# Optimization experiments

Hardware: AMD Instinct MI355X
Metric: run time of the kernel (lower is better)

## Reference

```python
import jax, jax.numpy as jnp
import numpy as np

N = 50000   # num_nodes
T = 24      # window_size
H = 64      # hidden_dim
HOR = 12    # horizon
E = 1600000 # num edges


def setup_inputs() -> dict:
    key = jax.random.key(0)
    ks = jax.random.split(key, 12)
    s = 1.0 / np.sqrt(H)
    u = lambda k, shape: jax.random.uniform(k, shape, jnp.float32, -s, s)
    return {
        "x": jax.random.normal(ks[0], (N, T), jnp.float32),
        "edge_index": jax.random.randint(ks[1], (2, E), 0, N, dtype=jnp.int32),
        "w_ih": u(ks[2], (3 * H, 1)),
        "w_hh": u(ks[3], (3 * H, H)),
        "b_ih": u(ks[4], (3 * H,)),
        "b_hh": u(ks[5], (3 * H,)),
        "gc1_w": u(ks[6], (H, H)),
        "gc1_b": u(ks[7], (H,)),
        "gc2_w": u(ks[8], (H, H)),
        "gc2_b": u(ks[9], (H,)),
        "fc_w": u(ks[10], (HOR, H)),
        "fc_b": u(ks[11], (HOR,)),
    }


def _gru_last(x, w_ih, w_hh, b_ih, b_hh):
    # x: [N, T] scalar-per-step input (input_size=1). Returns final hidden [N, H].
    h0 = jnp.zeros((x.shape[0], H), x.dtype)

    def step(h, xt):  # xt: [N]
        gi = xt[:, None] * w_ih[:, 0][None, :] + b_ih   # [N, 3H]
        gh = h @ w_hh.T + b_hh                          # [N, 3H]
        i_r, i_z, i_n = jnp.split(gi, 3, axis=-1)
        h_r, h_z, h_n = jnp.split(gh, 3, axis=-1)
        r = jax.nn.sigmoid(i_r + h_r)
        z = jax.nn.sigmoid(i_z + h_z)
        n = jnp.tanh(i_n + r * h_n)
        h = (1.0 - z) * n + z * h
        return h, None

    hT, _ = jax.lax.scan(step, h0, x.T)  # scan over time axis
    return hT


def _gcn_norm(edge_index, n):
    # PyG GCNConv: add self loops, symmetric D^-1/2 (A+I) D^-1/2 normalization.
    loops = jnp.arange(n, dtype=edge_index.dtype)
    src = jnp.concatenate([edge_index[0], loops])
    dst = jnp.concatenate([edge_index[1], loops])
    deg = jax.ops.segment_sum(jnp.ones(src.shape, jnp.float32), dst, num_segments=n)
    dinv = jnp.where(deg > 0, jax.lax.rsqrt(jnp.maximum(deg, 1e-12)), 0.0)
    return src, dst, dinv[src] * dinv[dst]


def _gcn(h, src, dst, norm, W, b, n):
    hw = h @ W.T                      # [N, H] linear transform first
    msg = hw[src] * norm[:, None]     # gather + edge weighting
    return jax.ops.segment_sum(msg, dst, num_segments=n) + b


def reference(x, edge_index, w_ih, w_hh, b_ih, b_hh, gc1_w, gc1_b, gc2_w, gc2_b, fc_w, fc_b):
    n = x.shape[0]
    h = _gru_last(x, w_ih, w_hh, b_ih, b_hh)            # [N, H] last GRU output
    src, dst, norm = _gcn_norm(edge_index, n)
    h = jax.nn.relu(_gcn(h, src, dst, norm, gc1_w, gc1_b, n))
    h = jax.nn.relu(_gcn(h, src, dst, norm, gc2_w, gc2_b, n))
    return h @ fc_w.T + fc_b                            # [N, HOR]
```

## Files before the change

### kernel.cpp

```cpp
#include <hip/hip_runtime.h>

#define NN 50000
#define TT 24
#define HH 64
#define HORZ 12
#define EE 1600000

#define GP 256
#define EP (EE / GP)
#define BK 784
#define NBG (BK * GP)
#define SCB (NBG / 512)
#define BKA ((NN + 63) / 64)

typedef __attribute__((ext_vector_type(8))) _Float16 f16x8;
typedef __attribute__((ext_vector_type(4))) float f32x4;

__device__ __forceinline__ float sigm(float x) {
  return __builtin_amdgcn_rcpf(1.f + __expf(-x));
}
__device__ __forceinline__ float tanh_f(float x) {
  return 1.f - 2.f * __builtin_amdgcn_rcpf(1.f + __expf(2.f * x));
}

__global__ void build_frags_kernel(const float* __restrict__ whh, const float* __restrict__ g1,
                                   const float* __restrict__ g2, const float* __restrict__ fcw,
                                   _Float16* __restrict__ frag) {
  int idx = blockIdx.x * 256 + threadIdx.x;
  if (idx >= 21504) return;
  const float* W;
  int rows, li;
  if (idx < 12288) { W = whh; rows = 192; li = idx; }
  else if (idx < 16384) { W = g1; rows = 64; li = idx - 12288; }
  else if (idx < 20480) { W = g2; rows = 64; li = idx - 16384; }
  else { W = fcw; rows = HORZ; li = idx - 20480; }
  int j = li & 7;
  int l = (li >> 3) & 63;
  int kf = (li >> 9) & 1;
  int nf = li >> 10;
  int col = 16 * nf + (l & 15);
  int k = 32 * kf + 8 * (l >> 4) + j;
  frag[idx] = (col < rows) ? (_Float16)W[col * 64 + k] : (_Float16)0.f;
}

__global__ __launch_bounds__(256) void p1_hist_kernel(const int* __restrict__ dst,
                                                      int* __restrict__ hist) {
  __shared__ int h[BK];
  int tid = threadIdx.x, g = blockIdx.x;
  for (int b = tid; b < BK; b += 256) h[b] = 0;
  __syncthreads();
  int e0 = g * EP;
  for (int i = tid; i < EP; i += 256) atomicAdd(&h[dst[e0 + i] >> 6], 1);
  __syncthreads();
  for (int b = tid; b < BK; b += 256) hist[b * GP + g] = h[b];
}

__global__ void scanA_kernel(const int* __restrict__ v, int* __restrict__ part) {
  __shared__ int s[512];
  int i = blockIdx.x * 512 + threadIdx.x;
  s[threadIdx.x] = v[i];
  __syncthreads();
  for (int off = 256; off > 0; off >>= 1) {
    if (threadIdx.x < off) s[threadIdx.x] += s[threadIdx.x + off];
    __syncthreads();
  }
  if (threadIdx.x == 0) part[blockIdx.x] = s[0];
}

__global__ void scanB_kernel(int* __restrict__ part) {
  __shared__ int s[512];
  int t = threadIdx.x;
  int v = (t < SCB) ? part[t] : 0;
  s[t] = v;
  __syncthreads();
  for (int off = 1; off < 512; off <<= 1) {
    int a = s[t];
    int b = (t >= off) ? s[t - off] : 0;
    __syncthreads();
    s[t] = a + b;
    __syncthreads();
  }
  if (t < SCB) part[t] = s[t] - v;
}

__global__ void scanC_kernel(int* __restrict__ cellbase, const int* __restrict__ part) {
  __shared__ int s[2][512];
  int tid = threadIdx.x;
  int i = blockIdx.x * 512 + tid;
  int x = cellbase[i];
  s[0][tid] = x;
  __syncthreads();
  int cur = 0;
  for (int off = 1; off < 512; off <<= 1) {
    int nxt = cur ^ 1;
    int val = s[cur][tid] + ((tid >= off) ? s[cur][tid - off] : 0);
    s[nxt][tid] = val;
    __syncthreads();
    cur = nxt;
  }
  cellbase[i] = part[blockIdx.x] + s[cur][tid] - x;
  if (i == 0) cellbase[NBG] = EE;
}

__global__ __launch_bounds__(256) void p2_scatter_kernel(
    const int* __restrict__ src, const int* __restrict__ dst,
    const int* __restrict__ cellbase, unsigned int* __restrict__ rec) {
  __shared__ int cur[BK];
  int tid = threadIdx.x, g = blockIdx.x;
  for (int b = tid; b < BK; b += 256) cur[b] = cellbase[b * GP + g];
  __syncthreads();
  int e0 = g * EP;
  for (int i = tid; i < EP; i += 256) {
    int e = e0 + i;
    int d = dst[e];
    int s = src[e];
    int p = atomicAdd(&cur[d >> 6], 1);
    rec[p] = ((unsigned)(d & 63) << 16) | (unsigned)s;
  }
}

__global__ __launch_bounds__(256) void sort2_kernel(
    const unsigned int* __restrict__ rec, const int* __restrict__ cellbase,
    unsigned short* __restrict__ csr, int* __restrict__ row_start,
    float* __restrict__ dinv) {
  __shared__ int cnt[64];
  __shared__ int cur[64];
  int b = blockIdx.x, tid = threadIdx.x;
  if (tid < 64) cnt[tid] = 0;
  __syncthreads();
  int e0 = cellbase[b * GP], e1 = cellbase[(b + 1) * GP];
  for (int e = e0 + tid; e < e1; e += 256) atomicAdd(&cnt[rec[e] >> 16], 1);
  __syncthreads();
  if (tid == 0) {
    int a = e0;
#pragma unroll
    for (int l = 0; l < 64; ++l) { int c = cnt[l]; cur[l] = a; a += c; }
  }
  __syncthreads();
  if (tid < 64) {
    int n = b * 64 + tid;
    if (n <= NN) row_start[n] = cur[tid];
    if (n < NN) dinv[n] = rsqrtf((float)(cnt[tid] + 1));
  }
  __syncthreads();
  for (int e = e0 + tid; e < e1; e += 256) {
    unsigned int r = rec[e];
    int p = atomicAdd(&cur[r >> 16], 1);
    csr[p] = (unsigned short)(r & 0xFFFFu);
  }
}

__global__ __launch_bounds__(256, 8) void gru_kernel(
    const float* __restrict__ x, const float* __restrict__ w_ih,
    const float* __restrict__ b_ih, const float* __restrict__ b_hh,
    const _Float16* __restrict__ wfrag, const _Float16* __restrict__ l1f,
    const float* __restrict__ dinv, _Float16* __restrict__ hw) {
  __shared__ __align__(16) _Float16 sh[2][16][72];
  __shared__ __align__(16) float xs[TT][16];

  const int tid = threadIdx.x;
  const int lane = tid & 63;
  const int w = tid >> 6;
  const int c = lane & 15;
  const int q = lane >> 4;
  const int d = 16 * w + c;

  f16x8 Br0 = *(const f16x8*)&wfrag[(((w)*2 + 0) * 64 + lane) * 8];
  f16x8 Br1 = *(const f16x8*)&wfrag[(((w)*2 + 1) * 64 + lane) * 8];
  f16x8 Bz0 = *(const f16x8*)&wfrag[(((4 + w) * 2 + 0) * 64 + lane) * 8];
  f16x8 Bz1 = *(const f16x8*)&wfrag[(((4 + w) * 2 + 1) * 64 + lane) * 8];
  f16x8 Bn0 = *(const f16x8*)&wfrag[(((8 + w) * 2 + 0) * 64 + lane) * 8];
  f16x8 Bn1 = *(const f16x8*)&wfrag[(((8 + w) * 2 + 1) * 64 + lane) * 8];

  const float wir = w_ih[d], wiz = w_ih[64 + d], win = w_ih[128 + d];
  const float arb = b_ih[d] + b_hh[d];
  const float azb = b_ih[64 + d] + b_hh[64 + d];
  const float bin = b_ih[128 + d];
  const float bhn = b_hh[128 + d];

  const int base = blockIdx.x * 16;

  for (int i = tid; i < 16 * TT; i += 256) {
    int nl = i / TT;
    int t = i - nl * TT;
    xs[t][nl] = x[(base + nl) * TT + t];
  }
  __syncthreads();

  float hreg[4] = {0.f, 0.f, 0.f, 0.f};

#pragma unroll 1
  for (int tp = 0; tp < TT / 2; ++tp) {
#pragma unroll
    for (int half = 0; half < 2; ++half) {
      const int t = 2 * tp + half;
      f32x4 ar = (f32x4){arb, arb, arb, arb};
      f32x4 az = (f32x4){azb, azb, azb, azb};
      f32x4 an = (f32x4){bhn, bhn, bhn, bhn};
      if (t > 0) {
        const _Float16* S = &sh[half ^ 1][0][0];
        f16x8 a0 = *(const f16x8*)&S[c * 72 + 8 * q];
        f16x8 a1 = *(const f16x8*)&S[c * 72 + 32 + 8 * q];
        ar = __builtin_amdgcn_mfma_f32_16x16x32_f16(a0, Br0, ar, 0, 0, 0);
        az = __builtin_amdgcn_mfma_f32_16x16x32_f16(a0, Bz0, az, 0, 0, 0);
        an = __builtin_amdgcn_mfma_f32_16x16x32_f16(a0, Bn0, an, 0, 0, 0);
        ar = __builtin_amdgcn_mfma_f32_16x16x32_f16(a1, Br1, ar, 0, 0, 0);
        az = __builtin_amdgcn_mfma_f32_16x16x32_f16(a1, Bz1, az, 0, 0, 0);
        an = __builtin_amdgcn_mfma_f32_16x16x32_f16(a1, Bn1, an, 0, 0, 0);
      }
      float4 xt = *(const float4*)&xs[t][4 * q];
      float xv[4] = {xt.x, xt.y, xt.z, xt.w};
#pragma unroll
      for (int r = 0; r < 4; ++r) {
        float rg = sigm(xv[r] * wir + ar[r]);
        float zg = sigm(xv[r] * wiz + az[r]);
        float nn = tanh_f(rg * an[r] + (xv[r] * win + bin));
        float hn = nn + zg * (hreg[r] - nn);
        hreg[r] = hn;
        sh[half][4 * q + r][d] = (_Float16)hn;
      }
      __syncthreads();
    }
  }

  f16x8 L0 = *(const f16x8*)&l1f[((w * 2 + 0) * 64 + lane) * 8];
  f16x8 L1 = *(const f16x8*)&l1f[((w * 2 + 1) * 64 + lane) * 8];
  {
    const _Float16* S = &sh[1][0][0];
    f16x8 a0 = *(const f16x8*)&S[c * 72 + 8 * q];
    f16x8 a1 = *(const f16x8*)&S[c * 72 + 32 + 8 * q];
    f32x4 acc = (f32x4){0.f, 0.f, 0.f, 0.f};
    acc = __builtin_amdgcn_mfma_f32_16x16x32_f16(a0, L0, acc, 0, 0, 0);
    acc = __builtin_amdgcn_mfma_f32_16x16x32_f16(a1, L1, acc, 0, 0, 0);
#pragma unroll
    for (int r = 0; r < 4; ++r) {
      int n = base + 4 * q + r;
      hw[n * 64 + d] = (_Float16)(acc[r] * dinv[n]);
    }
  }
}

__global__ __launch_bounds__(1024, 4) void agg_lin_kernel(
    const _Float16* __restrict__ hwp, const float* __restrict__ dinv,
    const int* __restrict__ row_start, const unsigned short* __restrict__ csr,
    const float* __restrict__ bias, const _Float16* __restrict__ l2f,
    _Float16* __restrict__ out) {
  __shared__ __align__(16) _Float16 h1[64][72];
  int tid = threadIdx.x, b = blockIdx.x;
  int wv = tid >> 6, lane = tid & 63;
  float bl = bias[lane];
#pragma unroll 1
  for (int k = 0; k < 4; ++k) {
    int row = wv * 4 + k;
    int n = b * 64 + row;
    float v = 0.f;
    if (n < NN) {
      int e0 = row_start[n], e1 = row_start[n + 1];
      float a0 = (float)hwp[n * 64 + lane];
      float a1 = 0.f, a2 = 0.f, a3 = 0.f;
      int e = e0;
      for (; e < e1 && (e & 7); ++e) a0 += (float)hwp[(int)csr[e] * 64 + lane];
      for (; e + 8 <= e1; e += 8) {
        uint4 pk = *(const uint4*)&csr[e];
        a0 += (float)hwp[(pk.x & 0xFFFF) * 64 + lane];
        a1 += (float)hwp[(pk.x >> 16) * 64 + lane];
        a2 += (float)hwp[(pk.y & 0xFFFF) * 64 + lane];
        a3 += (float)hwp[(pk.y >> 16) * 64 + lane];
        a0 += (float)hwp[(pk.z & 0xFFFF) * 64 + lane];
        a1 += (float)hwp[(pk.z >> 16) * 64 + lane];
        a2 += (float)hwp[(pk.w & 0xFFFF) * 64 + lane];
        a3 += (float)hwp[(pk.w >> 16) * 64 + lane];
      }
      for (; e < e1; ++e) a0 += (float)hwp[(int)csr[e] * 64 + lane];
      v = (a0 + a1 + a2 + a3) * dinv[n] + bl;
      v = v > 0.f ? v : 0.f;
    }
    h1[row][lane] = (_Float16)v;
  }
  __syncthreads();
  int g = wv >> 2, wq = wv & 3;
  int c = lane & 15, q = lane >> 4;
  f16x8 B0 = *(const f16x8*)&l2f[((wq * 2 + 0) * 64 + lane) * 8];
  f16x8 B1 = *(const f16x8*)&l2f[((wq * 2 + 1) * 64 + lane) * 8];
  f16x8 a0 = *(const f16x8*)&h1[16 * g + c][8 * q];
  f16x8 a1 = *(const f16x8*)&h1[16 * g + c][32 + 8 * q];
  f32x4 acc = (f32x4){0.f, 0.f, 0.f, 0.f};
  acc = __builtin_amdgcn_mfma_f32_16x16x32_f16(a0, B0, acc, 0, 0, 0);
  acc = __builtin_amdgcn_mfma_f32_16x16x32_f16(a1, B1, acc, 0, 0, 0);
#pragma unroll
  for (int r = 0; r < 4; ++r) {
    int n = b * 64 + 16 * g + 4 * q + r;
    if (n < NN) out[n * 64 + 16 * wq + c] = (_Float16)(acc[r] * dinv[n]);
  }
}

__global__ __launch_bounds__(1024, 4) void agg_fc_kernel(
    const _Float16* __restrict__ hwp, const float* __restrict__ dinv,
    const int* __restrict__ row_start, const unsigned short* __restrict__ csr,
    const float* __restrict__ bias, const _Float16* __restrict__ fcf,
    const float* __restrict__ fcb, float* __restrict__ out) {
  __shared__ __align__(16) _Float16 h1[64][72];
  int tid = threadIdx.x, b = blockIdx.x;
  int wv = tid >> 6, lane = tid & 63;
  float bl = bias[lane];
#pragma unroll 1
  for (int k = 0; k < 4; ++k) {
    int row = wv * 4 + k;
    int n = b * 64 + row;
    float v = 0.f;
    if (n < NN) {
      int e0 = row_start[n], e1 = row_start[n + 1];
      float a0 = (float)hwp[n * 64 + lane];
      float a1 = 0.f, a2 = 0.f, a3 = 0.f;
      int e = e0;
      for (; e < e1 && (e & 7); ++e) a0 += (float)hwp[(int)csr[e] * 64 + lane];
      for (; e + 8 <= e1; e += 8) {
        uint4 pk = *(const uint4*)&csr[e];
        a0 += (float)hwp[(pk.x & 0xFFFF) * 64 + lane];
        a1 += (float)hwp[(pk.x >> 16) * 64 + lane];
        a2 += (float)hwp[(pk.y & 0xFFFF) * 64 + lane];
        a3 += (float)hwp[(pk.y >> 16) * 64 + lane];
        a0 += (float)hwp[(pk.z & 0xFFFF) * 64 + lane];
        a1 += (float)hwp[(pk.z >> 16) * 64 + lane];
        a2 += (float)hwp[(pk.w & 0xFFFF) * 64 + lane];
        a3 += (float)hwp[(pk.w >> 16) * 64 + lane];
      }
      for (; e < e1; ++e) a0 += (float)hwp[(int)csr[e] * 64 + lane];
      v = (a0 + a1 + a2 + a3) * dinv[n] + bl;
      v = v > 0.f ? v : 0.f;
    }
    h1[row][lane] = (_Float16)v;
  }
  __syncthreads();
  if (wv < 4) {
    int g = wv;
    int c = lane & 15, q = lane >> 4;
    f16x8 B0 = *(const f16x8*)&fcf[(0 * 64 + lane) * 8];
    f16x8 B1 = *(const f16x8*)&fcf[(1 * 64 + lane) * 8];
    f16x8 a0 = *(const f16x8*)&h1[16 * g + c][8 * q];
    f16x8 a1 = *(const f16x8*)&h1[16 * g + c][32 + 8 * q];
    float bc = (c < HORZ) ? fcb[c] : 0.f;
    f32x4 acc = (f32x4){bc, bc, bc, bc};
    acc = __builtin_amdgcn_mfma_f32_16x16x32_f16(a0, B0, acc, 0, 0, 0);
    acc = __builtin_amdgcn_mfma_f32_16x16x32_f16(a1, B1, acc, 0, 0, 0);
    if (c < HORZ) {
#pragma unroll
      for (int r = 0; r < 4; ++r) {
        int n = b * 64 + 16 * g + 4 * q + r;
        if (n < NN) out[n * HORZ + c] = acc[r];
      }
    }
  }
}

extern "C" void kernel_launch(void* const* d_in, const int* in_sizes, int n_in,
                              void* d_out, int out_size, void* d_ws, size_t ws_size,
                              hipStream_t stream) {
  (void)in_sizes; (void)n_in; (void)out_size; (void)ws_size;
  const float* x = (const float*)d_in[0];
  const int* edge_index = (const int*)d_in[1];
  const float* w_ih = (const float*)d_in[2];
  const float* w_hh = (const float*)d_in[3];
  const float* b_ih = (const float*)d_in[4];
  const float* b_hh = (const float*)d_in[5];
  const float* gc1_w = (const float*)d_in[6];
  const float* gc1_b = (const float*)d_in[7];
  const float* gc2_w = (const float*)d_in[8];
  const float* gc2_b = (const float*)d_in[9];
  const float* fc_w = (const float*)d_in[10];
  const float* fc_b = (const float*)d_in[11];
  float* out = (float*)d_out;

  char* ws = (char*)d_ws;
  _Float16* wfrag = (_Float16*)ws;
  _Float16* l1f = wfrag + 12288;
  _Float16* l2f = l1f + 4096;
  _Float16* fcf = l2f + 4096;
  _Float16* hw1 = (_Float16*)(ws + 43008);
  _Float16* hw2 = hw1 + NN * 64;
  float* dinv = (float*)(hw2 + NN * 64);
  int* row_start = (int*)(dinv + NN);
  int* cellbase = row_start + 50240;
  int* part = cellbase + NBG + 4;
  unsigned int* rec = (unsigned int*)(part + 512);
  unsigned short* csr = (unsigned short*)(rec + EE);

  const int* esrc = edge_index;
  const int* edst = edge_index + EE;

  build_frags_kernel<<<84, 256, 0, stream>>>(w_hh, gc1_w, gc2_w, fc_w, wfrag);
  p1_hist_kernel<<<GP, 256, 0, stream>>>(edst, cellbase);
  scanA_kernel<<<SCB, 512, 0, stream>>>(cellbase, part);
  scanB_kernel<<<1, 512, 0, stream>>>(part);
  scanC_kernel<<<SCB, 512, 0, stream>>>(cellbase, part);
  p2_scatter_kernel<<<GP, 256, 0, stream>>>(esrc, edst, cellbase, rec);
  sort2_kernel<<<BK, 256, 0, stream>>>(rec, cellbase, csr, row_start, dinv);

  gru_kernel<<<NN / 16, 256, 0, stream>>>(x, w_ih, b_ih, b_hh, wfrag, l1f, dinv, hw1);
  agg_lin_kernel<<<BKA, 1024, 0, stream>>>(hw1, dinv, row_start, csr, gc1_b, l2f, hw2);
  agg_fc_kernel<<<BKA, 1024, 0, stream>>>(hw2, dinv, row_start, csr, gc2_b, fcf, fc_b, out);
}
```

Measured before the change: 276.3 us.

## Merge frag build into histogram kernel, transpose GRU MFMA, unroll gathers by 16

Folds the weight-fragment build kernel into the edge histogram kernel by adding extra blocks, which removes one launch. Swaps the MFMA operand order in the GRU so each lane holds four consecutive hidden dims of one node, turning per-element scalar LDS and global stores into packed 4-wide f16 stores and reading x once per step. Lowers the GRU occupancy hint from 8 to 5 and adds a 16-edge unrolled gather loop in both aggregation kernels to put more loads in flight. The per-lane bias and weight arrays raise register use, which the new launch bound permits.

```diff
diff --git a/kernel.cpp b/kernel.cpp
--- a/kernel.cpp
+++ b/kernel.cpp
@@ -14,6 +14,7 @@
 #define BKA ((NN + 63) / 64)
 
 typedef __attribute__((ext_vector_type(8))) _Float16 f16x8;
+typedef __attribute__((ext_vector_type(4))) _Float16 f16x4;
 typedef __attribute__((ext_vector_type(4))) float f32x4;
 
 __device__ __forceinline__ float sigm(float x) {
@@ -23,30 +24,32 @@
   return 1.f - 2.f * __builtin_amdgcn_rcpf(1.f + __expf(2.f * x));
 }
 
-__global__ void build_frags_kernel(const float* __restrict__ whh, const float* __restrict__ g1,
-                                   const float* __restrict__ g2, const float* __restrict__ fcw,
-                                   _Float16* __restrict__ frag) {
-  int idx = blockIdx.x * 256 + threadIdx.x;
-  if (idx >= 21504) return;
-  const float* W;
-  int rows, li;
-  if (idx < 12288) { W = whh; rows = 192; li = idx; }
-  else if (idx < 16384) { W = g1; rows = 64; li = idx - 12288; }
-  else if (idx < 20480) { W = g2; rows = 64; li = idx - 16384; }
-  else { W = fcw; rows = HORZ; li = idx - 20480; }
-  int j = li & 7;
-  int l = (li >> 3) & 63;
-  int kf = (li >> 9) & 1;
-  int nf = li >> 10;
-  int col = 16 * nf + (l & 15);
-  int k = 32 * kf + 8 * (l >> 4) + j;
-  frag[idx] = (col < rows) ? (_Float16)W[col * 64 + k] : (_Float16)0.f;
-}
-
-__global__ __launch_bounds__(256) void p1_hist_kernel(const int* __restrict__ dst,
-                                                      int* __restrict__ hist) {
+__global__ __launch_bounds__(256) void p1_frags_kernel(
+    const int* __restrict__ dst, int* __restrict__ hist,
+    const float* __restrict__ whh, const float* __restrict__ g1,
+    const float* __restrict__ g2, const float* __restrict__ fcw,
+    _Float16* __restrict__ frag) {
+  int bid = blockIdx.x;
+  if (bid >= GP) {
+    int idx = (bid - GP) * 256 + threadIdx.x;
+    if (idx >= 21504) return;
+    const float* W;
+    int rows, li;
+    if (idx < 12288) { W = whh; rows = 192; li = idx; }
+    else if (idx < 16384) { W = g1; rows = 64; li = idx - 12288; }
+    else if (idx < 20480) { W = g2; rows = 64; li = idx - 16384; }
+    else { W = fcw; rows = HORZ; li = idx - 20480; }
+    int j = li & 7;
+    int l = (li >> 3) & 63;
+    int kf = (li >> 9) & 1;
+    int nf = li >> 10;
+    int col = 16 * nf + (l & 15);
+    int k = 32 * kf + 8 * (l >> 4) + j;
+    frag[idx] = (col < rows) ? (_Float16)W[col * 64 + k] : (_Float16)0.f;
+    return;
+  }
   __shared__ int h[BK];
-  int tid = threadIdx.x, g = blockIdx.x;
+  int tid = threadIdx.x, g = bid;
   for (int b = tid; b < BK; b += 256) h[b] = 0;
   __syncthreads();
   int e0 = g * EP;
@@ -150,7 +153,7 @@
   }
 }
 
-__global__ __launch_bounds__(256, 8) void gru_kernel(
+__global__ __launch_bounds__(256, 5) void gru_kernel(
     const float* __restrict__ x, const float* __restrict__ w_ih,
     const float* __restrict__ b_ih, const float* __restrict__ b_hh,
     const _Float16* __restrict__ wfrag, const _Float16* __restrict__ l1f,
@@ -163,20 +166,24 @@
   const int w = tid >> 6;
   const int c = lane & 15;
   const int q = lane >> 4;
-  const int d = 16 * w + c;
-
-  f16x8 Br0 = *(const f16x8*)&wfrag[(((w)*2 + 0) * 64 + lane) * 8];
-  f16x8 Br1 = *(const f16x8*)&wfrag[(((w)*2 + 1) * 64 + lane) * 8];
-  f16x8 Bz0 = *(const f16x8*)&wfrag[(((4 + w) * 2 + 0) * 64 + lane) * 8];
-  f16x8 Bz1 = *(const f16x8*)&wfrag[(((4 + w) * 2 + 1) * 64 + lane) * 8];
-  f16x8 Bn0 = *(const f16x8*)&wfrag[(((8 + w) * 2 + 0) * 64 + lane) * 8];
-  f16x8 Bn1 = *(const f16x8*)&wfrag[(((8 + w) * 2 + 1) * 64 + lane) * 8];
-
-  const float wir = w_ih[d], wiz = w_ih[64 + d], win = w_ih[128 + d];
-  const float arb = b_ih[d] + b_hh[d];
-  const float azb = b_ih[64 + d] + b_hh[64 + d];
-  const float bin = b_ih[128 + d];
-  const float bhn = b_hh[128 + d];
+
+  f16x8 Ar0 = *(const f16x8*)&wfrag[(((w)*2 + 0) * 64 + lane) * 8];
+  f16x8 Ar1 = *(const f16x8*)&wfrag[(((w)*2 + 1) * 64 + lane) * 8];
+  f16x8 Az0 = *(const f16x8*)&wfrag[(((4 + w) * 2 + 0) * 64 + lane) * 8];
+  f16x8 Az1 = *(const f16x8*)&wfrag[(((4 + w) * 2 + 1) * 64 + lane) * 8];
+  f16x8 An0 = *(const f16x8*)&wfrag[(((8 + w) * 2 + 0) * 64 + lane) * 8];
+  f16x8 An1 = *(const f16x8*)&wfrag[(((8 + w) * 2 + 1) * 64 + lane) * 8];
+
+  float wir[4], wiz[4], win[4], arb[4], azb[4], binc[4], bhnc[4];
+#pragma unroll
+  for (int r = 0; r < 4; ++r) {
+    int dd = 16 * w + 4 * q + r;
+    wir[r] = w_ih[dd]; wiz[r] = w_ih[64 + dd]; win[r] = w_ih[128 + dd];
+    arb[r] = b_ih[dd] + b_hh[dd];
+    azb[r] = b_ih[64 + dd] + b_hh[64 + dd];
+    binc[r] = b_ih[128 + dd];
+    bhnc[r] = b_hh[128 + dd];
+  }
 
   const int base = blockIdx.x * 16;
 
@@ -194,49 +201,50 @@
 #pragma unroll
     for (int half = 0; half < 2; ++half) {
       const int t = 2 * tp + half;
-      f32x4 ar = (f32x4){arb, arb, arb, arb};
-      f32x4 az = (f32x4){azb, azb, azb, azb};
-      f32x4 an = (f32x4){bhn, bhn, bhn, bhn};
+      f32x4 ar = (f32x4){arb[0], arb[1], arb[2], arb[3]};
+      f32x4 az = (f32x4){azb[0], azb[1], azb[2], azb[3]};
+      f32x4 an = (f32x4){bhnc[0], bhnc[1], bhnc[2], bhnc[3]};
       if (t > 0) {
         const _Float16* S = &sh[half ^ 1][0][0];
-        f16x8 a0 = *(const f16x8*)&S[c * 72 + 8 * q];
-        f16x8 a1 = *(const f16x8*)&S[c * 72 + 32 + 8 * q];
-        ar = __builtin_amdgcn_mfma_f32_16x16x32_f16(a0, Br0, ar, 0, 0, 0);
-        az = __builtin_amdgcn_mfma_f32_16x16x32_f16(a0, Bz0, az, 0, 0, 0);
-        an = __builtin_amdgcn_mfma_f32_16x16x32_f16(a0, Bn0, an, 0, 0, 0);
-        ar = __builtin_amdgcn_mfma_f32_16x16x32_f16(a1, Br1, ar, 0, 0, 0);
-        az = __builtin_amdgcn_mfma_f32_16x16x32_f16(a1, Bz1, az, 0, 0, 0);
-        an = __builtin_amdgcn_mfma_f32_16x16x32_f16(a1, Bn1, an, 0, 0, 0);
-      }
-      float4 xt = *(const float4*)&xs[t][4 * q];
-      float xv[4] = {xt.x, xt.y, xt.z, xt.w};
+        f16x8 b0 = *(const f16x8*)&S[c * 72 + 8 * q];
+        f16x8 b1 = *(const f16x8*)&S[c * 72 + 32 + 8 * q];
+        ar = __builtin_amdgcn_mfma_f32_16x16x32_f16(Ar0, b0, ar, 0, 0, 0);
+        az = __builtin_amdgcn_mfma_f32_16x16x32_f16(Az0, b0, az, 0, 0, 0);
+        an = __builtin_amdgcn_mfma_f32_16x16x32_f16(An0, b0, an, 0, 0, 0);
+        ar = __builtin_amdgcn_mfma_f32_16x16x32_f16(Ar1, b1, ar, 0, 0, 0);
+        az = __builtin_amdgcn_mfma_f32_16x16x32_f16(Az1, b1, az, 0, 0, 0);
+        an = __builtin_amdgcn_mfma_f32_16x16x32_f16(An1, b1, an, 0, 0, 0);
+      }
+      float xv = xs[t][c];
+      f16x4 hpack;
 #pragma unroll
       for (int r = 0; r < 4; ++r) {
-        float rg = sigm(xv[r] * wir + ar[r]);
-        float zg = sigm(xv[r] * wiz + az[r]);
-        float nn = tanh_f(rg * an[r] + (xv[r] * win + bin));
+        float rg = sigm(xv * wir[r] + ar[r]);
+        float zg = sigm(xv * wiz[r] + az[r]);
+        float nn = tanh_f(rg * an[r] + (xv * win[r] + binc[r]));
         float hn = nn + zg * (hreg[r] - nn);
         hreg[r] = hn;
-        sh[half][4 * q + r][d] = (_Float16)hn;
-      }
+        hpack[r] = (_Float16)hn;
+      }
+      *(f16x4*)&sh[half][c][16 * w + 4 * q] = hpack;
       __syncthreads();
     }
   }
 
-  f16x8 L0 = *(const f16x8*)&l1f[((w * 2 + 0) * 64 + lane) * 8];
-  f16x8 L1 = *(const f16x8*)&l1f[((w * 2 + 1) * 64 + lane) * 8];
   {
+    f16x8 L0 = *(const f16x8*)&l1f[((w * 2 + 0) * 64 + lane) * 8];
+    f16x8 L1 = *(const f16x8*)&l1f[((w * 2 + 1) * 64 + lane) * 8];
     const _Float16* S = &sh[1][0][0];
-    f16x8 a0 = *(const f16x8*)&S[c * 72 + 8 * q];
-    f16x8 a1 = *(const f16x8*)&S[c * 72 + 32 + 8 * q];
+    f16x8 b0 = *(const f16x8*)&S[c * 72 + 8 * q];
+    f16x8 b1 = *(const f16x8*)&S[c * 72 + 32 + 8 * q];
     f32x4 acc = (f32x4){0.f, 0.f, 0.f, 0.f};
-    acc = __builtin_amdgcn_mfma_f32_16x16x32_f16(a0, L0, acc, 0, 0, 0);
-    acc = __builtin_amdgcn_mfma_f32_16x16x32_f16(a1, L1, acc, 0, 0, 0);
-#pragma unroll
-    for (int r = 0; r < 4; ++r) {
-      int n = base + 4 * q + r;
-      hw[n * 64 + d] = (_Float16)(acc[r] * dinv[n]);
-    }
+    acc = __builtin_amdgcn_mfma_f32_16x16x32_f16(L0, b0, acc, 0, 0, 0);
+    acc = __builtin_amdgcn_mfma_f32_16x16x32_f16(L1, b1, acc, 0, 0, 0);
+    float dn = dinv[base + c];
+    f16x4 opack;
+#pragma unroll
+    for (int r = 0; r < 4; ++r) opack[r] = (_Float16)(acc[r] * dn);
+    *(f16x4*)&hw[(base + c) * 64 + 16 * w + 4 * q] = opack;
   }
 }
 
@@ -260,6 +268,26 @@
       float a1 = 0.f, a2 = 0.f, a3 = 0.f;
       int e = e0;
       for (; e < e1 && (e & 7); ++e) a0 += (float)hwp[(int)csr[e] * 64 + lane];
+      for (; e + 16 <= e1; e += 16) {
+        uint4 p0 = *(const uint4*)&csr[e];
+        uint4 p1 = *(const uint4*)&csr[e + 8];
+        a0 += (float)hwp[(p0.x & 0xFFFF) * 64 + lane];
+        a1 += (float)hwp[(p0.x >> 16) * 64 + lane];
+        a2 += (float)hwp[(p0.y & 0xFFFF) * 64 + lane];
+        a3 += (float)hwp[(p0.y >> 16) * 64 + lane];
+        a0 += (float)hwp[(p0.z & 0xFFFF) * 64 + lane];
+        a1 += (float)hwp[(p0.z >> 16) * 64 + lane];
+        a2 += (float)hwp[(p0.w & 0xFFFF) * 64 + lane];
+        a3 += (float)hwp[(p0.w >> 16) * 64 + lane];
+        a0 += (float)hwp[(p1.x & 0xFFFF) * 64 + lane];
+        a1 += (float)hwp[(p1.x >> 16) * 64 + lane];
+        a2 += (float)hwp[(p1.y & 0xFFFF) * 64 + lane];
+        a3 += (float)hwp[(p1.y >> 16) * 64 + lane];
+        a0 += (float)hwp[(p1.z & 0xFFFF) * 64 + lane];
+        a1 += (float)hwp[(p1.z >> 16) * 64 + lane];
+        a2 += (float)hwp[(p1.w & 0xFFFF) * 64 + lane];
+        a3 += (float)hwp[(p1.w >> 16) * 64 + lane];
+      }
       for (; e + 8 <= e1; e += 8) {
         uint4 pk = *(const uint4*)&csr[e];
         a0 += (float)hwp[(pk.x & 0xFFFF) * 64 + lane];
@@ -314,6 +342,26 @@
       float a1 = 0.f, a2 = 0.f, a3 = 0.f;
       int e = e0;
       for (; e < e1 && (e & 7); ++e) a0 += (float)hwp[(int)csr[e] * 64 + lane];
+      for (; e + 16 <= e1; e += 16) {
+        uint4 p0 = *(const uint4*)&csr[e];
+        uint4 p1 = *(const uint4*)&csr[e + 8];
+        a0 += (float)hwp[(p0.x & 0xFFFF) * 64 + lane];
+        a1 += (float)hwp[(p0.x >> 16) * 64 + lane];
+        a2 += (float)hwp[(p0.y & 0xFFFF) * 64 + lane];
+        a3 += (float)hwp[(p0.y >> 16) * 64 + lane];
+        a0 += (float)hwp[(p0.z & 0xFFFF) * 64 + lane];
+        a1 += (float)hwp[(p0.z >> 16) * 64 + lane];
+        a2 += (float)hwp[(p0.w & 0xFFFF) * 64 + lane];
+        a3 += (float)hwp[(p0.w >> 16) * 64 + lane];
+        a0 += (float)hwp[(p1.x & 0xFFFF) * 64 + lane];
+        a1 += (float)hwp[(p1.x >> 16) * 64 + lane];
+        a2 += (float)hwp[(p1.y & 0xFFFF) * 64 + lane];
+        a3 += (float)hwp[(p1.y >> 16) * 64 + lane];
+        a0 += (float)hwp[(p1.z & 0xFFFF) * 64 + lane];
+        a1 += (float)hwp[(p1.z >> 16) * 64 + lane];
+        a2 += (float)hwp[(p1.w & 0xFFFF) * 64 + lane];
+        a3 += (float)hwp[(p1.w >> 16) * 64 + lane];
+      }
       for (; e + 8 <= e1; e += 8) {
         uint4 pk = *(const uint4*)&csr[e];
         a0 += (float)hwp[(pk.x & 0xFFFF) * 64 + lane];
@@ -388,8 +436,7 @@
   const int* esrc = edge_index;
   const int* edst = edge_index + EE;
 
-  build_frags_kernel<<<84, 256, 0, stream>>>(w_hh, gc1_w, gc2_w, fc_w, wfrag);
-  p1_hist_kernel<<<GP, 256, 0, stream>>>(edst, cellbase);
+  p1_frags_kernel<<<GP + 84, 256, 0, stream>>>(edst, cellbase, w_hh, gc1_w, gc2_w, fc_w, wfrag);
   scanA_kernel<<<SCB, 512, 0, stream>>>(cellbase, part);
   scanB_kernel<<<1, 512, 0, stream>>>(part);
   scanC_kernel<<<SCB, 512, 0, stream>>>(cellbase, part);
```

After: 240.8 us. 1.15x faster.
